# Kernel tuning notes

Hardware: AMD Instinct MI355X
Metric: run time of the kernel (lower is better)

The kernel has to match this reference:

```python
import jax, jax.numpy as jnp
import numpy as np


def setup_inputs() -> dict:
    key = jax.random.key(0)
    k0, k1, k2, k3, k4 = jax.random.split(key, 5)
    n, c, s, h, w = 4, 128, 31, 32, 22
    x = jax.random.normal(k0, (n, c, s, h, w), dtype=jnp.float32)
    # 1x1 conv to a single channel == per-pixel dot over channels + scalar bias
    scale = 1.0 / np.sqrt(c).astype(np.float32)
    w1 = jax.random.normal(k1, (c,), dtype=jnp.float32) * scale
    b1 = jax.random.normal(k2, (), dtype=jnp.float32) * 0.01
    w2 = jax.random.normal(k3, (c,), dtype=jnp.float32) * scale
    b2 = jax.random.normal(k4, (), dtype=jnp.float32) * 0.01
    return {"x": x, "w1": w1, "b1": b1, "w2": w2, "b2": b2, "top_k": 16}


def reference(x, w1, b1, w2, b2, top_k):
    n, c, s, h, w = x.shape
    hw = h * w
    ns = n * (s - 1)
    # adjacent-frame pairs; 1x1 conv (C->1) as channel contraction
    X0 = jnp.einsum('ncshw,c->nshw', x[:, :, : s - 1], w1) + b1  # (n, s-1, h, w)
    X1 = jnp.einsum('ncshw,c->nshw', x[:, :, 1:], w2) + b2       # (n, s-1, h, w)
    X0 = X0.reshape(ns, hw)
    X1 = X1.reshape(ns, hw)
    # outer-product scores per frame pair, softmax over last dim
    attention = jax.nn.softmax(X0[:, :, None] * X1[:, None, :], axis=2)  # (ns, hw, hw)
    # top-k values along last dim -> (ns, hw, k); torch .view(ns, k, h, w)
    # is a raw row-major reinterpretation, so a plain reshape is faithful.
    vals, _ = jax.lax.top_k(attention, top_k)
    vals = vals.reshape(n, s - 1, top_k, h, w)
    # trans_out: (n, s-1, k, h, w) -> (n, k, s-1, h, w)
    return jnp.transpose(vals, (0, 2, 1, 3, 4))
```

## Files before the change

kernel.cpp:

```cpp
#include <hip/hip_runtime.h>
#include <math.h>

#define NB   4
#define C    128
#define S    31
#define HW   704
#define T    30
#define NS   120
#define K    16

__global__ __launch_bounds__(256) void conv_kernel(
    const float* __restrict__ x,
    const float* __restrict__ w1, const float* __restrict__ b1p,
    const float* __restrict__ w2, const float* __restrict__ b2p,
    float* __restrict__ A, float* __restrict__ B) {
  const int tid  = threadIdx.x;
  const int lane = tid & 63;
  const int cg   = tid >> 6;
  const int g    = blockIdx.x * 64 + lane;
  const int fr   = g / 176;
  const int f4   = g % 176;
  const int sf   = fr % S;
  const int n    = fr / S;

  const float4* xp =
      (const float4*)(x + (((size_t)(n * C + cg * 32) * S + sf) * HW)) + f4;
  float4 a1 = make_float4(0.f, 0.f, 0.f, 0.f);
  float4 a2 = make_float4(0.f, 0.f, 0.f, 0.f);
#pragma unroll
  for (int c = 0; c < 32; ++c) {
    float4 xv = xp[(size_t)c * (S * HW / 4)];
    const float wa = w1[cg * 32 + c];
    const float wb = w2[cg * 32 + c];
    a1.x = fmaf(xv.x, wa, a1.x); a1.y = fmaf(xv.y, wa, a1.y);
    a1.z = fmaf(xv.z, wa, a1.z); a1.w = fmaf(xv.w, wa, a1.w);
    a2.x = fmaf(xv.x, wb, a2.x); a2.y = fmaf(xv.y, wb, a2.y);
    a2.z = fmaf(xv.z, wb, a2.z); a2.w = fmaf(xv.w, wb, a2.w);
  }
  __shared__ float4 s1[4][64];
  __shared__ float4 s2[4][64];
  s1[cg][lane] = a1;
  s2[cg][lane] = a2;
  __syncthreads();
  if (tid < 64) {
    float4 r1 = s1[0][tid], r2 = s2[0][tid];
#pragma unroll
    for (int u = 1; u < 4; ++u) {
      float4 t1 = s1[u][tid], t2 = s2[u][tid];
      r1.x += t1.x; r1.y += t1.y; r1.z += t1.z; r1.w += t1.w;
      r2.x += t2.x; r2.y += t2.y; r2.z += t2.z; r2.w += t2.w;
    }
    const float bb1 = b1p[0], bb2 = b2p[0];
    r1.x += bb1; r1.y += bb1; r1.z += bb1; r1.w += bb1;
    r2.x += bb2; r2.y += bb2; r2.z += bb2; r2.w += bb2;
    if (sf < T)
      ((float4*)(A + (size_t)(n * T + sf) * HW))[f4] = r1;
    if (sf >= 1)
      ((float4*)(B + (size_t)(n * T + sf - 1) * HW))[f4] = r2;
  }
}

__global__ __launch_bounds__(64) void select_kernel(
    const float* __restrict__ B,
    float* __restrict__ btop, float* __restrict__ bbot) {
  const int i    = blockIdx.x;
  const int lane = threadIdx.x;
  const float* __restrict__ bi = B + i * HW;

  float vt[11], vb[11];
#pragma unroll
  for (int j = 0; j < 11; ++j) {
    const float v = bi[j * 64 + lane];
    vt[j] = v;
    vb[j] = v;
  }

#pragma unroll 1
  for (int r = 0; r < K; ++r) {
    float lmT = vt[0], lmB = vb[0];
#pragma unroll
    for (int j = 1; j < 11; ++j) {
      lmT = fmaxf(lmT, vt[j]);
      lmB = fminf(lmB, vb[j]);
    }
    float gT = lmT, gB = lmB;
#pragma unroll
    for (int off = 1; off < 64; off <<= 1) {
      gT = fmaxf(gT, __shfl_xor(gT, off, 64));
      gB = fminf(gB, __shfl_xor(gB, off, 64));
    }
    const unsigned long long mT = __ballot(lmT == gT);
    const unsigned long long mB = __ballot(lmB == gB);
    if (lane == (int)(__ffsll(mT) - 1)) {
      bool done = false;
#pragma unroll
      for (int j = 0; j < 11; ++j) {
        const bool hit = (!done) && (vt[j] == gT);
        vt[j] = hit ? -INFINITY : vt[j];
        done  = done || hit;
      }
    }
    if (lane == (int)(__ffsll(mB) - 1)) {
      bool done = false;
#pragma unroll
      for (int j = 0; j < 11; ++j) {
        const bool hit = (!done) && (vb[j] == gB);
        vb[j] = hit ? INFINITY : vb[j];
        done  = done || hit;
      }
    }
    if (lane == 0) {
      btop[i * K + r] = gT;
      bbot[i * K + r] = gB;
    }
  }
}

__global__ __launch_bounds__(256) void softmax_topk_kernel(
    const float* __restrict__ A, const float* __restrict__ B,
    const float* __restrict__ btop, const float* __restrict__ bbot,
    float* __restrict__ out) {
  const int lane = threadIdx.x & 63;
  const int wid  = blockIdx.x * 4 + (threadIdx.x >> 6);
  const int i    = wid / 176;
  const int rb   = wid % 176;

  const float st0 = btop[i * K];
  const float sb0 = bbot[i * K];
  const float L2E = 1.4426950408889634f;
  float av[4], a2[4], nm[4], part[4];
#pragma unroll
  for (int u = 0; u < 4; ++u) {
    av[u]   = A[i * HW + rb + u * 176];
    a2[u]   = av[u] * L2E;
    nm[u]   = -((av[u] >= 0.f) ? av[u] * st0 : av[u] * sb0) * L2E;
    part[u] = 0.f;
  }

  const float* __restrict__ bi = B + i * HW;
#pragma unroll
  for (int j = 0; j < 11; ++j) {
    const float bv = bi[j * 64 + lane];
#pragma unroll
    for (int u = 0; u < 4; ++u)
      part[u] += __builtin_amdgcn_exp2f(fmaf(a2[u], bv, nm[u]));
  }
#pragma unroll
  for (int off = 1; off < 64; off <<= 1) {
#pragma unroll
    for (int u = 0; u < 4; ++u)
      part[u] += __shfl_xor(part[u], off, 64);
  }

  if (lane < K) {
    const int n  = i / T;
    const int t  = i % T;
    float* obase = out + (((size_t)n * K) * T + t) * HW;
    const float tv = btop[i * K + lane];
    const float bv = bbot[i * K + lane];
#pragma unroll
    for (int u = 0; u < 4; ++u) {
      const int r = rb + u * 176;
      const float sel = (av[u] >= 0.f) ? tv : bv;
      const float val = __builtin_amdgcn_exp2f(fmaf(a2[u], sel, nm[u])) / part[u];
      obase[(size_t)(r / 44) * (T * HW) + (r % 44) * K + lane] = val;
    }
  }
}

extern "C" void kernel_launch(void* const* d_in, const int* in_sizes, int n_in,
                              void* d_out, int out_size, void* d_ws, size_t ws_size,
                              hipStream_t stream) {
  (void)in_sizes; (void)n_in; (void)out_size; (void)ws_size;
  const float* x  = (const float*)d_in[0];
  const float* w1 = (const float*)d_in[1];
  const float* b1 = (const float*)d_in[2];
  const float* w2 = (const float*)d_in[3];
  const float* b2 = (const float*)d_in[4];
  float* out = (float*)d_out;

  float* A    = (float*)d_ws;
  float* B    = A + NS * HW;
  float* btop = B + NS * HW;
  float* bbot = btop + NS * K;

  conv_kernel<<<341, 256, 0, stream>>>(x, w1, b1, w2, b2, A, B);
  select_kernel<<<NS, 64, 0, stream>>>(B, btop, bbot);
  softmax_topk_kernel<<<5280, 256, 0, stream>>>(A, B, btop, bbot, out);
}
```

Before: 115.3 us.

## Fuse conv and per-frame top/bottom-k selection into one kernel per frame

Merges the channel-contraction conv kernel and the B top/bottom-16 selection kernel into a single kernel with one 768-thread block per frame. The reduced B frame stays in shared memory and one wavefront runs the selection from there, so a kernel launch and the global reload of B are removed. The cost is that only 124 blocks are launched, which lowers parallelism for the memory-bound conv phase, and the selection runs serially at the end of each block while the other wavefronts sit idle.

```diff
diff --git a/kernel.cpp b/kernel.cpp
--- a/kernel.cpp
+++ b/kernel.cpp
@@ -8,20 +8,23 @@
 #define T    30
 #define NS   120
 #define K    16
+#define NFR  124
 
-__global__ __launch_bounds__(256) void conv_kernel(
+__global__ __launch_bounds__(768) void conv_select_kernel(
     const float* __restrict__ x,
     const float* __restrict__ w1, const float* __restrict__ b1p,
     const float* __restrict__ w2, const float* __restrict__ b2p,
-    float* __restrict__ A, float* __restrict__ B) {
-  const int tid  = threadIdx.x;
-  const int lane = tid & 63;
-  const int cg   = tid >> 6;
-  const int g    = blockIdx.x * 64 + lane;
-  const int fr   = g / 176;
-  const int f4   = g % 176;
-  const int sf   = fr % S;
-  const int n    = fr / S;
+    float* __restrict__ A, float* __restrict__ B,
+    float* __restrict__ btop, float* __restrict__ bbot) {
+  const int tid = threadIdx.x;
+  const int wv    = __builtin_amdgcn_readfirstlane(tid) >> 6;
+  const int cg    = wv / 3;
+  const int local = tid - cg * 192;
+  const bool act  = local < 176;
+  const int f4    = act ? local : 175;
+  const int fr    = blockIdx.x;
+  const int sf    = fr % S;
+  const int n     = fr / S;
 
   const float4* xp =
       (const float4*)(x + (((size_t)(n * C + cg * 32) * S + sf) * HW)) + f4;
@@ -37,12 +40,16 @@
     a2.x = fmaf(xv.x, wb, a2.x); a2.y = fmaf(xv.y, wb, a2.y);
     a2.z = fmaf(xv.z, wb, a2.z); a2.w = fmaf(xv.w, wb, a2.w);
   }
-  __shared__ float4 s1[4][64];
-  __shared__ float4 s2[4][64];
-  s1[cg][lane] = a1;
-  s2[cg][lane] = a2;
+
+  __shared__ float4 s1[4][176];
+  __shared__ float4 s2[4][176];
+  if (act) {
+    s1[cg][f4] = a1;
+    s2[cg][f4] = a2;
+  }
   __syncthreads();
-  if (tid < 64) {
+
+  if (tid < 176) {
     float4 r1 = s1[0][tid], r2 = s2[0][tid];
 #pragma unroll
     for (int u = 1; u < 4; ++u) {
@@ -54,64 +61,61 @@
     r1.x += bb1; r1.y += bb1; r1.z += bb1; r1.w += bb1;
     r2.x += bb2; r2.y += bb2; r2.z += bb2; r2.w += bb2;
     if (sf < T)
-      ((float4*)(A + (size_t)(n * T + sf) * HW))[f4] = r1;
+      ((float4*)(A + (size_t)(n * T + sf) * HW))[tid] = r1;
     if (sf >= 1)
-      ((float4*)(B + (size_t)(n * T + sf - 1) * HW))[f4] = r2;
+      ((float4*)(B + (size_t)(n * T + sf - 1) * HW))[tid] = r2;
+    s2[0][tid] = r2;
   }
-}
+  __syncthreads();
 
-__global__ __launch_bounds__(64) void select_kernel(
-    const float* __restrict__ B,
-    float* __restrict__ btop, float* __restrict__ bbot) {
-  const int i    = blockIdx.x;
-  const int lane = threadIdx.x;
-  const float* __restrict__ bi = B + i * HW;
-
-  float vt[11], vb[11];
+  if (tid < 64 && sf >= 1) {
+    const int i = n * T + sf - 1;
+    const float* bs = (const float*)&s2[0][0];
+    float vt[11], vb[11];
 #pragma unroll
-  for (int j = 0; j < 11; ++j) {
-    const float v = bi[j * 64 + lane];
-    vt[j] = v;
-    vb[j] = v;
-  }
-
+    for (int j = 0; j < 11; ++j) {
+      const float v = bs[j * 64 + tid];
+      vt[j] = v;
+      vb[j] = v;
+    }
 #pragma unroll 1
-  for (int r = 0; r < K; ++r) {
-    float lmT = vt[0], lmB = vb[0];
+    for (int r = 0; r < K; ++r) {
+      float lmT = vt[0], lmB = vb[0];
 #pragma unroll
-    for (int j = 1; j < 11; ++j) {
-      lmT = fmaxf(lmT, vt[j]);
-      lmB = fminf(lmB, vb[j]);
-    }
-    float gT = lmT, gB = lmB;
+      for (int j = 1; j < 11; ++j) {
+        lmT = fmaxf(lmT, vt[j]);
+        lmB = fminf(lmB, vb[j]);
+      }
+      float gT = lmT, gB = lmB;
 #pragma unroll
-    for (int off = 1; off < 64; off <<= 1) {
-      gT = fmaxf(gT, __shfl_xor(gT, off, 64));
-      gB = fminf(gB, __shfl_xor(gB, off, 64));
-    }
-    const unsigned long long mT = __ballot(lmT == gT);
-    const unsigned long long mB = __ballot(lmB == gB);
-    if (lane == (int)(__ffsll(mT) - 1)) {
-      bool done = false;
+      for (int off = 1; off < 64; off <<= 1) {
+        gT = fmaxf(gT, __shfl_xor(gT, off, 64));
+        gB = fminf(gB, __shfl_xor(gB, off, 64));
+      }
+      const unsigned long long mT = __ballot(lmT == gT);
+      const unsigned long long mB = __ballot(lmB == gB);
+      if (tid == (int)(__ffsll(mT) - 1)) {
+        bool done = false;
 #pragma unroll
-      for (int j = 0; j < 11; ++j) {
-        const bool hit = (!done) && (vt[j] == gT);
-        vt[j] = hit ? -INFINITY : vt[j];
-        done  = done || hit;
+        for (int j = 0; j < 11; ++j) {
+          const bool hit = (!done) && (vt[j] == gT);
+          vt[j] = hit ? -INFINITY : vt[j];
+          done  = done || hit;
+        }
       }
-    }
-    if (lane == (int)(__ffsll(mB) - 1)) {
-      bool done = false;
+      if (tid == (int)(__ffsll(mB) - 1)) {
+        bool done = false;
 #pragma unroll
-      for (int j = 0; j < 11; ++j) {
-        const bool hit = (!done) && (vb[j] == gB);
-        vb[j] = hit ? INFINITY : vb[j];
-        done  = done || hit;
+        for (int j = 0; j < 11; ++j) {
+          const bool hit = (!done) && (vb[j] == gB);
+          vb[j] = hit ? INFINITY : vb[j];
+          done  = done || hit;
+        }
       }
-    }
-    if (lane == 0) {
-      btop[i * K + r] = gT;
-      bbot[i * K + r] = gB;
+      if (tid == 0) {
+        btop[i * K + r] = gT;
+        bbot[i * K + r] = gB;
+      }
     }
   }
 }
@@ -184,7 +188,7 @@
   float* btop = B + NS * HW;
   float* bbot = btop + NS * K;
 
-  conv_kernel<<<341, 256, 0, stream>>>(x, w1, b1, w2, b2, A, B);
-  select_kernel<<<NS, 64, 0, stream>>>(B, btop, bbot);
+  conv_select_kernel<<<NFR, 768, 0, stream>>>(x, w1, b1, w2, b2,
+                                              A, B, btop, bbot);
   softmax_topk_kernel<<<5280, 256, 0, stream>>>(A, B, btop, bbot, out);
 }
```

Result: no change. 114.9 us (-0.3%).
